# Performance work log

Hardware: AMD Instinct MI355X
Metric: run time of the kernel (lower is better)

Reference implementation:

```python
import jax, jax.numpy as jnp
import numpy as np
import math

HIDDEN = 2048
HEADS = 16
HEAD_DIM = HIDDEN // HEADS
SEQ = 2048
BATCH = 1
THRESH = 0.7


def setup_inputs() -> dict:
    key = jax.random.key(0)
    ks = jax.random.split(key, 9)
    init = lambda k, shape: (jax.random.normal(k, shape, dtype=jnp.float32) * 0.02)
    return {
        "hidden_states": jax.random.normal(ks[0], (BATCH, SEQ, HIDDEN), dtype=jnp.float32),
        "Wq": init(ks[1], (HIDDEN, HIDDEN)), "bq": jnp.zeros((HIDDEN,), jnp.float32),
        "Wk": init(ks[2], (HIDDEN, HIDDEN)), "bk": jnp.zeros((HIDDEN,), jnp.float32),
        "Wv": init(ks[3], (HIDDEN, HIDDEN)), "bv": jnp.zeros((HIDDEN,), jnp.float32),
        "Wo": init(ks[4], (HIDDEN, HIDDEN)), "bo": jnp.zeros((HIDDEN,), jnp.float32),
        "truth_gate": jnp.full((1,), THRESH, jnp.float32),
        "balance_gate": jnp.full((1,), THRESH, jnp.float32),
        "order_gate": jnp.full((1,), THRESH, jnp.float32),
        "justice_gate": jnp.full((1,), THRESH, jnp.float32),
        "harmony_gate": jnp.full((1,), THRESH, jnp.float32),
    }


def reference(hidden_states, Wq, bq, Wk, bk, Wv, bv, Wo, bo,
              truth_gate, balance_gate, order_gate, justice_gate, harmony_gate):
    B, S, D = hidden_states.shape
    H, hd = HEADS, HEAD_DIM
    # projections -> [B, H, S, hd]
    def proj(W, b):
        return (hidden_states @ W.T + b).reshape(B, S, H, hd).transpose(0, 2, 1, 3)
    q, k, v = proj(Wq, bq), proj(Wk, bk), proj(Wv, bv)

    scores = jnp.einsum('bhqd,bhkd->bhqk', q, k) / math.sqrt(hd)  # [B,H,S,S]

    # truth: penalize by key norm, broadcast over query axis? No -- k_norm is [B,H,S,1],
    # matching torch broadcasting: per-QUERY-row constant (k indexed like q rows).
    truth_penalty = jax.nn.sigmoid(truth_gate) * (jnp.linalg.norm(k, axis=-1, keepdims=True) * 0.01)

    # balance: row entropy of softmax(scores)
    logp = jax.nn.log_softmax(scores, axis=-1)
    entropy = -jnp.sum(jnp.exp(logp) * logp, axis=-1, keepdims=True)  # [B,H,S,1]
    balance_adjustment = jax.nn.sigmoid(balance_gate) * (entropy / math.log(S) * 0.1)

    # order: position bias over the LAST (key) axis, shape [1,1,S] in torch -> broadcasts on key dim
    position_bias = jnp.arange(S, dtype=jnp.float32) / S  # [S]
    order_bonus = jax.nn.sigmoid(order_gate) * (position_bias * 0.05)  # broadcasts over bhq,k

    # justice: pull scores toward their row mean
    mean_score = scores.mean(axis=-1, keepdims=True)
    justice_adjustment = jax.nn.sigmoid(justice_gate) * ((mean_score - scores) * 0.1)

    # harmony: negative mean abs diff along key axis, per row
    smoothness = -jnp.abs(scores[..., 1:] - scores[..., :-1]).mean(axis=-1, keepdims=True)
    harmony_smooth = jax.nn.sigmoid(harmony_gate) * (smoothness * 0.1)

    scores = scores - truth_penalty + balance_adjustment + order_bonus + justice_adjustment + harmony_smooth

    attn = jax.nn.softmax(scores, axis=-1)
    out = jnp.einsum('bhqk,bhkd->bhqd', attn, v)  # [B,H,S,hd]
    out = out.transpose(0, 2, 1, 3).reshape(B, S, D)
    return out @ Wo.T + bo
```

## Files before the change

### kernel.cpp

```cpp
#include <hip/hip_runtime.h>

typedef __bf16 bf16x8 __attribute__((ext_vector_type(8)));
typedef __bf16 bf16x4 __attribute__((ext_vector_type(4)));
typedef float f32x4 __attribute__((ext_vector_type(4)));

typedef const __attribute__((address_space(1))) void* gas_t;
typedef __attribute__((address_space(3))) void* las_t;

static constexpr int DIM = 2048;
static constexpr size_t MAT = (size_t)DIM * DIM;

__device__ __forceinline__ float sigmoidf_(float x) { return 1.f / (1.f + __expf(-x)); }

__global__ void cvt_kernel(const float* __restrict__ x, const float* __restrict__ wq,
                           const float* __restrict__ wk, const float* __restrict__ wv,
                           const float* __restrict__ wo, __bf16* __restrict__ dst) {
  const float* s;
  switch (blockIdx.y) {
    case 0: s = x; break;
    case 1: s = wq; break;
    case 2: s = wk; break;
    case 3: s = wv; break;
    default: s = wo; break;
  }
  __bf16* d = dst + (size_t)blockIdx.y * MAT;
  size_t i = ((size_t)blockIdx.x * 256 + threadIdx.x) * 4;
  float4 v = *(const float4*)(s + i);
  bf16x4 ov;
  ov[0] = (__bf16)v.x; ov[1] = (__bf16)v.y; ov[2] = (__bf16)v.z; ov[3] = (__bf16)v.w;
  *(bf16x4*)(d + i) = ov;
}

template <bool F32OUT>
__device__ __forceinline__ void gemm128(const __bf16* __restrict__ A, const __bf16* __restrict__ B,
                                        const float* __restrict__ bias, bool bias_row, float scale,
                                        void* __restrict__ Cout, int mtile, int ntile,
                                        __bf16* Asm, __bf16* Bsm) {
  const int t = threadIdx.x, lane = t & 63, w = t >> 6;
  const int wrow = (w >> 1) * 64, wcol = (w & 1) * 64;
  const int rbase = mtile * 128, cbase = ntile * 128;
  f32x4 acc[4][4] = {};

  for (int k0 = 0; k0 < DIM; k0 += 32) {
    __syncthreads();
#pragma unroll
    for (int i = 0; i < 2; ++i) {
      const int o = i * 4096 + w * 1024 + lane * 16;
      const int r = o >> 6;
      const int ke = (o & 63) >> 1;
      __builtin_amdgcn_global_load_lds((gas_t)(A + (size_t)(rbase + r) * DIM + k0 + ke),
                                       (las_t)(Asm + (o >> 1)), 16, 0, 0);
      __builtin_amdgcn_global_load_lds((gas_t)(B + (size_t)(cbase + r) * DIM + k0 + ke),
                                       (las_t)(Bsm + (o >> 1)), 16, 0, 0);
    }
    __syncthreads();

    bf16x8 af[4], bf[4];
#pragma unroll
    for (int i = 0; i < 4; ++i)
      af[i] = *(const bf16x8*)(Asm + (wrow + i * 16 + (lane & 15)) * 32 + (lane >> 4) * 8);
#pragma unroll
    for (int j = 0; j < 4; ++j)
      bf[j] = *(const bf16x8*)(Bsm + (wcol + j * 16 + (lane & 15)) * 32 + (lane >> 4) * 8);
#pragma unroll
    for (int i = 0; i < 4; ++i)
#pragma unroll
      for (int j = 0; j < 4; ++j)
        acc[i][j] = __builtin_amdgcn_mfma_f32_16x16x32_bf16(af[i], bf[j], acc[i][j], 0, 0, 0);
  }

#pragma unroll
  for (int i = 0; i < 4; ++i)
#pragma unroll
    for (int j = 0; j < 4; ++j)
#pragma unroll
      for (int r = 0; r < 4; ++r) {
        const int row = rbase + wrow + i * 16 + (lane >> 4) * 4 + r;
        const int col = cbase + wcol + j * 16 + (lane & 15);
        float v = acc[i][j][r] + (bias_row ? bias[row] : bias[col]);
        v *= scale;
        if (F32OUT)
          ((float*)Cout)[(size_t)row * DIM + col] = v;
        else
          ((__bf16*)Cout)[(size_t)row * DIM + col] = (__bf16)v;
      }
}

__global__ __launch_bounds__(256, 2) void qkv_kernel(
    const __bf16* __restrict__ Xb, const __bf16* __restrict__ Wqb, const __bf16* __restrict__ Wkb,
    const __bf16* __restrict__ Wvb, const float* __restrict__ bq, const float* __restrict__ bk,
    const float* __restrict__ bv, const float* __restrict__ jgate, __bf16* __restrict__ Qo,
    __bf16* __restrict__ Ko, __bf16* __restrict__ Vto) {
  __shared__ __bf16 Asm[128 * 32];
  __shared__ __bf16 Bsm[128 * 32];
  const int sel = blockIdx.x >> 4, nt = blockIdx.x & 15, mt = blockIdx.y;
  const __bf16 *A, *B;
  const float* bias;
  __bf16* C;
  bool brow = false;
  float sc = 1.f;
  if (sel == 0) {
    A = Xb; B = Wqb; bias = bq; C = Qo;
    sc = (1.f - 0.1f * sigmoidf_(jgate[0])) * 0.08838834764831843f;
  } else if (sel == 1) {
    A = Xb; B = Wkb; bias = bk; C = Ko;
  } else {
    A = Wvb; B = Xb; bias = bv; C = Vto; brow = true;
  }
  gemm128<false>(A, B, bias, brow, sc, C, mt, nt, Asm, Bsm);
}

__global__ __launch_bounds__(256, 2) void outproj_kernel(const __bf16* __restrict__ Ab,
                                                         const __bf16* __restrict__ Wob,
                                                         const float* __restrict__ bo,
                                                         float* __restrict__ Cout) {
  __shared__ __bf16 Asm[128 * 32];
  __shared__ __bf16 Bsm[128 * 32];
  gemm128<true>(Ab, Wob, bo, false, 1.f, Cout, blockIdx.y, blockIdx.x, Asm, Bsm);
}

__global__ __launch_bounds__(512) void attn_kernel(const __bf16* __restrict__ Q,
                                                   const __bf16* __restrict__ Kg,
                                                   const __bf16* __restrict__ VT,
                                                   const float* __restrict__ ogate,
                                                   __bf16* __restrict__ O) {
  __shared__ __bf16 Ks[2][4 * 64 * 32];
  __shared__ __bf16 Vs[2][2 * 128 * 32];
  __shared__ __bf16 Ps[8 * 16 * 72];
  const int t = threadIdx.x, lane = t & 63, w = t >> 6;
  const int h = blockIdx.y, qt = blockIdx.x;
  const float beta = sigmoidf_(ogate[0]) * 0.05f / 2048.0f;

  const int rs8 = (((lane >> 4) ^ ((lane >> 1) & 3)) & 3) * 8;

  const int qrow = qt * 128 + w * 16 + (lane & 15);
  bf16x8 qf[4];
#pragma unroll
  for (int c = 0; c < 4; ++c)
    qf[c] = *(const bf16x8*)(Q + (size_t)qrow * DIM + h * 128 + c * 32 + (lane >> 4) * 8);

  f32x4 oacc[8] = {};
  float m_r[4], l_r[4];
#pragma unroll
  for (int r = 0; r < 4; ++r) { m_r[r] = -1e30f; l_r[r] = 0.f; }

  auto stage = [&](int buf, int kt) {
#pragma unroll
    for (int i = 0; i < 2; ++i) {
      const int o = i * 8192 + w * 1024 + lane * 16;
      const int oz = o ^ (((o >> 7) & 3) << 4);
      const int ke = (oz & 63) >> 1;
      const int c = oz >> 12, key = (oz & 4095) >> 6;
      __builtin_amdgcn_global_load_lds(
          (gas_t)(Kg + (size_t)(kt + key) * DIM + h * 128 + c * 32 + ke),
          (las_t)(&Ks[buf][0] + (o >> 1)), 16, 0, 0);
      const int cc = oz >> 13, d = (oz & 8191) >> 6;
      __builtin_amdgcn_global_load_lds(
          (gas_t)(VT + (size_t)(h * 128 + d) * DIM + kt + cc * 32 + ke),
          (las_t)(&Vs[buf][0] + (o >> 1)), 16, 0, 0);
    }
  };

  stage(0, 0);
  int p = 0;
  for (int kt = 0; kt < 2048; kt += 64) {
    __syncthreads();
    if (kt + 64 < 2048) stage(p ^ 1, kt + 64);

    f32x4 s[4];
#pragma unroll
    for (int j = 0; j < 4; ++j) {
      f32x4 a = {};
#pragma unroll
      for (int c = 0; c < 4; ++c) {
        bf16x8 kf = *(const bf16x8*)(&Ks[p][0] + c * 2048 + (j * 16 + (lane & 15)) * 32 + rs8);
        a = __builtin_amdgcn_mfma_f32_16x16x32_bf16(qf[c], kf, a, 0, 0, 0);
      }
      s[j] = a;
    }
#pragma unroll
    for (int j = 0; j < 4; ++j) {
      const float pb = beta * (float)(kt + j * 16 + (lane & 15));
#pragma unroll
      for (int r = 0; r < 4; ++r) s[j][r] += pb;
    }
    float rmax[4];
#pragma unroll
    for (int r = 0; r < 4; ++r)
      rmax[r] = fmaxf(fmaxf(s[0][r], s[1][r]), fmaxf(s[2][r], s[3][r]));
#pragma unroll
    for (int msk = 1; msk < 16; msk <<= 1)
#pragma unroll
      for (int r = 0; r < 4; ++r) rmax[r] = fmaxf(rmax[r], __shfl_xor(rmax[r], msk, 64));

    float al[4];
#pragma unroll
    for (int r = 0; r < 4; ++r) {
      const float mn = fmaxf(m_r[r], rmax[r]);
      al[r] = __expf(m_r[r] - mn);
      m_r[r] = mn;
    }
#pragma unroll
    for (int j = 0; j < 4; ++j)
#pragma unroll
      for (int r = 0; r < 4; ++r) s[j][r] = __expf(s[j][r] - m_r[r]);

    float rs[4];
#pragma unroll
    for (int r = 0; r < 4; ++r) rs[r] = (s[0][r] + s[1][r]) + (s[2][r] + s[3][r]);
#pragma unroll
    for (int msk = 1; msk < 16; msk <<= 1)
#pragma unroll
      for (int r = 0; r < 4; ++r) rs[r] += __shfl_xor(rs[r], msk, 64);
#pragma unroll
    for (int r = 0; r < 4; ++r) l_r[r] = l_r[r] * al[r] + rs[r];
#pragma unroll
    for (int d = 0; d < 8; ++d)
#pragma unroll
      for (int r = 0; r < 4; ++r) oacc[d][r] *= al[r];

    {
      __bf16* pw = Ps + w * 1152;
#pragma unroll
      for (int j = 0; j < 4; ++j)
#pragma unroll
        for (int r = 0; r < 4; ++r)
          pw[((lane >> 4) * 4 + r) * 72 + j * 16 + (lane & 15)] = (__bf16)s[j][r];
    }

#pragma unroll
    for (int cc = 0; cc < 2; ++cc) {
      bf16x8 pa = *(const bf16x8*)(Ps + w * 1152 + (lane & 15) * 72 + cc * 32 + (lane >> 4) * 8);
#pragma unroll
      for (int d = 0; d < 8; ++d) {
        bf16x8 vf = *(const bf16x8*)(&Vs[p][0] + cc * 4096 + (d * 16 + (lane & 15)) * 32 + rs8);
        oacc[d] = __builtin_amdgcn_mfma_f32_16x16x32_bf16(pa, vf, oacc[d], 0, 0, 0);
      }
    }
    p ^= 1;
  }

#pragma unroll
  for (int d = 0; d < 8; ++d)
#pragma unroll
    for (int r = 0; r < 4; ++r) {
      const int row = qt * 128 + w * 16 + (lane >> 4) * 4 + r;
      const int col = h * 128 + d * 16 + (lane & 15);
      O[(size_t)row * DIM + col] = (__bf16)(oacc[d][r] / l_r[r]);
    }
}

extern "C" void kernel_launch(void* const* d_in, const int* in_sizes, int n_in,
                              void* d_out, int out_size, void* d_ws, size_t ws_size,
                              hipStream_t stream) {
  const float* X  = (const float*)d_in[0];
  const float* Wq = (const float*)d_in[1];
  const float* bq = (const float*)d_in[2];
  const float* Wk = (const float*)d_in[3];
  const float* bk = (const float*)d_in[4];
  const float* Wv = (const float*)d_in[5];
  const float* bv = (const float*)d_in[6];
  const float* Wo = (const float*)d_in[7];
  const float* bo = (const float*)d_in[8];
  const float* order_g   = (const float*)d_in[11];
  const float* justice_g = (const float*)d_in[12];

  __bf16* wsb = (__bf16*)d_ws;
  __bf16* Xb  = wsb + 0 * MAT;
  __bf16* Wqb = wsb + 1 * MAT;
  __bf16* Wkb = wsb + 2 * MAT;
  __bf16* Wvb = wsb + 3 * MAT;
  __bf16* Wob = wsb + 4 * MAT;
  __bf16* Qb  = wsb + 5 * MAT;
  __bf16* Kb  = wsb + 6 * MAT;
  __bf16* VTb = wsb + 7 * MAT;
  __bf16* Ab  = Xb;

  cvt_kernel<<<dim3(4096, 5), 256, 0, stream>>>(X, Wq, Wk, Wv, Wo, wsb);
  qkv_kernel<<<dim3(48, 16), 256, 0, stream>>>(Xb, Wqb, Wkb, Wvb, bq, bk, bv, justice_g,
                                               Qb, Kb, VTb);
  attn_kernel<<<dim3(16, 16), 512, 0, stream>>>(Qb, Kb, VTb, order_g, Ab);
  outproj_kernel<<<dim3(16, 16), 256, 0, stream>>>(Ab, Wob, bo, (float*)d_out);
}
```

Baseline: 315.5 us.

## Split attention over key halves with separate merge kernel

Splits the key sequence into two halves along a new grid dimension, doubling the attention grid from 256 to 512 blocks so the GPU's compute units are better occupied. Each half writes unnormalized fp32 partial outputs plus row max and sum, and a new merge kernel combines them into the bf16 attention output. It also swaps the padded P tile in shared memory for an XOR-swizzled layout. The cost is extra fp32 global traffic and an additional kernel launch. Partial buffers reuse the output buffer and workspace regions of weights that have already been consumed (Wq and Wv).

Result: no change. 318.1 us (+0.8%).

```diff
diff --git a/kernel.cpp b/kernel.cpp
--- a/kernel.cpp
+++ b/kernel.cpp
@@ -123,12 +123,15 @@
                                                    const __bf16* __restrict__ Kg,
                                                    const __bf16* __restrict__ VT,
                                                    const float* __restrict__ ogate,
-                                                   __bf16* __restrict__ O) {
+                                                   float* __restrict__ Od,
+                                                   float* __restrict__ Ow,
+                                                   float* __restrict__ ml) {
   __shared__ __bf16 Ks[2][4 * 64 * 32];
   __shared__ __bf16 Vs[2][2 * 128 * 32];
-  __shared__ __bf16 Ps[8 * 16 * 72];
+  __shared__ __bf16 Ps[8 * 16 * 64];
   const int t = threadIdx.x, lane = t & 63, w = t >> 6;
-  const int h = blockIdx.y, qt = blockIdx.x;
+  const int h = blockIdx.y, qt = blockIdx.x, s = blockIdx.z;
+  const int kt0 = s * 1024, kt1 = kt0 + 1024;
   const float beta = sigmoidf_(ogate[0]) * 0.05f / 2048.0f;
 
   const int rs8 = (((lane >> 4) ^ ((lane >> 1) & 3)) & 3) * 8;
@@ -154,20 +157,20 @@
       __builtin_amdgcn_global_load_lds(
           (gas_t)(Kg + (size_t)(kt + key) * DIM + h * 128 + c * 32 + ke),
           (las_t)(&Ks[buf][0] + (o >> 1)), 16, 0, 0);
-      const int cc = oz >> 13, d = (oz & 8191) >> 6;
+      const int d = (o & 8191) >> 6;
       __builtin_amdgcn_global_load_lds(
-          (gas_t)(VT + (size_t)(h * 128 + d) * DIM + kt + cc * 32 + ke),
+          (gas_t)(VT + (size_t)(h * 128 + d) * DIM + kt + i * 32 + ke),
           (las_t)(&Vs[buf][0] + (o >> 1)), 16, 0, 0);
     }
   };
 
-  stage(0, 0);
+  stage(0, kt0);
   int p = 0;
-  for (int kt = 0; kt < 2048; kt += 64) {
+  for (int kt = kt0; kt < kt1; kt += 64) {
     __syncthreads();
-    if (kt + 64 < 2048) stage(p ^ 1, kt + 64);
-
-    f32x4 s[4];
+    if (kt + 64 < kt1) stage(p ^ 1, kt + 64);
+
+    f32x4 sc[4];
 #pragma unroll
     for (int j = 0; j < 4; ++j) {
       f32x4 a = {};
@@ -176,18 +179,18 @@
         bf16x8 kf = *(const bf16x8*)(&Ks[p][0] + c * 2048 + (j * 16 + (lane & 15)) * 32 + rs8);
         a = __builtin_amdgcn_mfma_f32_16x16x32_bf16(qf[c], kf, a, 0, 0, 0);
       }
-      s[j] = a;
+      sc[j] = a;
     }
 #pragma unroll
     for (int j = 0; j < 4; ++j) {
       const float pb = beta * (float)(kt + j * 16 + (lane & 15));
 #pragma unroll
-      for (int r = 0; r < 4; ++r) s[j][r] += pb;
+      for (int r = 0; r < 4; ++r) sc[j][r] += pb;
     }
     float rmax[4];
 #pragma unroll
     for (int r = 0; r < 4; ++r)
-      rmax[r] = fmaxf(fmaxf(s[0][r], s[1][r]), fmaxf(s[2][r], s[3][r]));
+      rmax[r] = fmaxf(fmaxf(sc[0][r], sc[1][r]), fmaxf(sc[2][r], sc[3][r]));
 #pragma unroll
     for (int msk = 1; msk < 16; msk <<= 1)
 #pragma unroll
@@ -203,11 +206,11 @@
 #pragma unroll
     for (int j = 0; j < 4; ++j)
 #pragma unroll
-      for (int r = 0; r < 4; ++r) s[j][r] = __expf(s[j][r] - m_r[r]);
+      for (int r = 0; r < 4; ++r) sc[j][r] = __expf(sc[j][r] - m_r[r]);
 
     float rs[4];
 #pragma unroll
-    for (int r = 0; r < 4; ++r) rs[r] = (s[0][r] + s[1][r]) + (s[2][r] + s[3][r]);
+    for (int r = 0; r < 4; ++r) rs[r] = (sc[0][r] + sc[1][r]) + (sc[2][r] + sc[3][r]);
 #pragma unroll
     for (int msk = 1; msk < 16; msk <<= 1)
 #pragma unroll
@@ -220,17 +223,20 @@
       for (int r = 0; r < 4; ++r) oacc[d][r] *= al[r];
 
     {
-      __bf16* pw = Ps + w * 1152;
+      __bf16* pw = Ps + w * 1024;
 #pragma unroll
       for (int j = 0; j < 4; ++j)
 #pragma unroll
-        for (int r = 0; r < 4; ++r)
-          pw[((lane >> 4) * 4 + r) * 72 + j * 16 + (lane & 15)] = (__bf16)s[j][r];
+        for (int r = 0; r < 4; ++r) {
+          const int q = (lane >> 4) * 4 + r;
+          pw[(q * 64 + j * 16 + (lane & 15)) ^ ((q & 7) << 3)] = (__bf16)sc[j][r];
+        }
     }
 
 #pragma unroll
     for (int cc = 0; cc < 2; ++cc) {
-      bf16x8 pa = *(const bf16x8*)(Ps + w * 1152 + (lane & 15) * 72 + cc * 32 + (lane >> 4) * 8);
+      const int pe = (w * 1024 + (lane & 15) * 64 + cc * 32 + (lane >> 4) * 8) ^ ((lane & 7) << 3);
+      bf16x8 pa = *(const bf16x8*)(Ps + pe);
 #pragma unroll
       for (int d = 0; d < 8; ++d) {
         bf16x8 vf = *(const bf16x8*)(&Vs[p][0] + cc * 4096 + (d * 16 + (lane & 15)) * 32 + rs8);
@@ -240,14 +246,43 @@
     p ^= 1;
   }
 
+  float* Op = (s == 0) ? Od : Ow;
 #pragma unroll
   for (int d = 0; d < 8; ++d)
 #pragma unroll
     for (int r = 0; r < 4; ++r) {
       const int row = qt * 128 + w * 16 + (lane >> 4) * 4 + r;
       const int col = h * 128 + d * 16 + (lane & 15);
-      O[(size_t)row * DIM + col] = (__bf16)(oacc[d][r] / l_r[r]);
-    }
+      Op[(size_t)row * DIM + col] = oacc[d][r];
+    }
+  if ((lane & 15) == 0) {
+#pragma unroll
+    for (int r = 0; r < 4; ++r) {
+      const int row = qt * 128 + w * 16 + (lane >> 4) * 4 + r;
+      ml[s * 32768 + h * 2048 + row] = m_r[r];
+      ml[65536 + s * 32768 + h * 2048 + row] = l_r[r];
+    }
+  }
+}
+
+__global__ void merge_kernel(const float* __restrict__ O1, const float* __restrict__ O2,
+                             const float* __restrict__ ml, __bf16* __restrict__ Ab) {
+  const size_t i = ((size_t)blockIdx.x * 256 + threadIdx.x) * 4;
+  const int row = (int)(i >> 11), col = (int)(i & 2047), h = col >> 7;
+  const int mi = h * 2048 + row;
+  const float m1 = ml[mi], m2 = ml[32768 + mi];
+  const float l1 = ml[65536 + mi], l2 = ml[98304 + mi];
+  const float M = fmaxf(m1, m2);
+  const float a1 = __expf(m1 - M), a2 = __expf(m2 - M);
+  const float inv = 1.f / (a1 * l1 + a2 * l2);
+  const float4 o1 = *(const float4*)(O1 + i);
+  const float4 o2 = *(const float4*)(O2 + i);
+  bf16x4 ov;
+  ov[0] = (__bf16)((a1 * o1.x + a2 * o2.x) * inv);
+  ov[1] = (__bf16)((a1 * o1.y + a2 * o2.y) * inv);
+  ov[2] = (__bf16)((a1 * o1.z + a2 * o2.z) * inv);
+  ov[3] = (__bf16)((a1 * o1.w + a2 * o2.w) * inv);
+  *(bf16x4*)(Ab + i) = ov;
 }
 
 extern "C" void kernel_launch(void* const* d_in, const int* in_sizes, int n_in,
@@ -275,10 +310,14 @@
   __bf16* Kb  = wsb + 6 * MAT;
   __bf16* VTb = wsb + 7 * MAT;
   __bf16* Ab  = Xb;
+  float* Opart0 = (float*)d_out;
+  float* Opart1 = (float*)(wsb + 1 * MAT);
+  float* mlbuf  = (float*)(wsb + 3 * MAT);
 
   cvt_kernel<<<dim3(4096, 5), 256, 0, stream>>>(X, Wq, Wk, Wv, Wo, wsb);
   qkv_kernel<<<dim3(48, 16), 256, 0, stream>>>(Xb, Wqb, Wkb, Wvb, bq, bk, bv, justice_g,
                                                Qb, Kb, VTb);
-  attn_kernel<<<dim3(16, 16), 512, 0, stream>>>(Qb, Kb, VTb, order_g, Ab);
+  attn_kernel<<<dim3(16, 16, 2), 512, 0, stream>>>(Qb, Kb, VTb, order_g, Opart0, Opart1, mlbuf);
+  merge_kernel<<<dim3(4096), 256, 0, stream>>>(Opart0, Opart1, mlbuf, Ab);
   outproj_kernel<<<dim3(16, 16), 256, 0, stream>>>(Ab, Wob, bo, (float*)d_out);
 }
```

## Pipeline GEMM loads four-deep and streamline the attention softmax loop

Applied to the files above, without the earlier changes.

The shared 128x128 GEMM used by the QKV and output projections now keeps a four-buffer LDS ring. It issues async global-to-LDS loads three K-steps ahead and waits on explicit vmcnt counts with a single barrier per step, instead of load-then-sync every iteration. The attention kernel raises wave priority around its MFMA blocks and skips the running-max rescale when no row max increased. It also replaces the padded P scratch with an XOR-swizzled 64-wide layout to avoid LDS bank conflicts. The GEMM ring quadruples LDS per block, which may limit occupancy, and the hand-counted vmcnt waits depend on exactly four loads per stage.

New measurement: 360.9 us. +14.4%, slower.

```diff
diff --git a/kernel.cpp b/kernel.cpp
--- a/kernel.cpp
+++ b/kernel.cpp
@@ -41,32 +41,46 @@
   const int rbase = mtile * 128, cbase = ntile * 128;
   f32x4 acc[4][4] = {};
 
-  for (int k0 = 0; k0 < DIM; k0 += 32) {
-    __syncthreads();
+  auto stage = [&](int buf, int k0) {
 #pragma unroll
     for (int i = 0; i < 2; ++i) {
       const int o = i * 4096 + w * 1024 + lane * 16;
       const int r = o >> 6;
       const int ke = (o & 63) >> 1;
       __builtin_amdgcn_global_load_lds((gas_t)(A + (size_t)(rbase + r) * DIM + k0 + ke),
-                                       (las_t)(Asm + (o >> 1)), 16, 0, 0);
+                                       (las_t)(Asm + buf * 4096 + (o >> 1)), 16, 0, 0);
       __builtin_amdgcn_global_load_lds((gas_t)(B + (size_t)(cbase + r) * DIM + k0 + ke),
-                                       (las_t)(Bsm + (o >> 1)), 16, 0, 0);
-    }
-    __syncthreads();
+                                       (las_t)(Bsm + buf * 4096 + (o >> 1)), 16, 0, 0);
+    }
+  };
+
+  stage(0, 0);
+  stage(1, 32);
+  stage(2, 64);
+  int buf = 0;
+  for (int k0 = 0; k0 < DIM; k0 += 32) {
+    if (k0 + 64 < DIM)      asm volatile("s_waitcnt vmcnt(8)" ::: "memory");
+    else if (k0 + 32 < DIM) asm volatile("s_waitcnt vmcnt(4)" ::: "memory");
+    else                    asm volatile("s_waitcnt vmcnt(0)" ::: "memory");
+    __builtin_amdgcn_s_barrier();
+    if (k0 + 96 < DIM) {
+      int sb = buf + 3; if (sb >= 4) sb -= 4;
+      stage(sb, k0 + 96);
+    }
 
     bf16x8 af[4], bf[4];
 #pragma unroll
     for (int i = 0; i < 4; ++i)
-      af[i] = *(const bf16x8*)(Asm + (wrow + i * 16 + (lane & 15)) * 32 + (lane >> 4) * 8);
+      af[i] = *(const bf16x8*)(Asm + buf * 4096 + (wrow + i * 16 + (lane & 15)) * 32 + (lane >> 4) * 8);
 #pragma unroll
     for (int j = 0; j < 4; ++j)
-      bf[j] = *(const bf16x8*)(Bsm + (wcol + j * 16 + (lane & 15)) * 32 + (lane >> 4) * 8);
+      bf[j] = *(const bf16x8*)(Bsm + buf * 4096 + (wcol + j * 16 + (lane & 15)) * 32 + (lane >> 4) * 8);
 #pragma unroll
     for (int i = 0; i < 4; ++i)
 #pragma unroll
       for (int j = 0; j < 4; ++j)
         acc[i][j] = __builtin_amdgcn_mfma_f32_16x16x32_bf16(af[i], bf[j], acc[i][j], 0, 0, 0);
+    buf = (buf + 1) & 3;
   }
 
 #pragma unroll
@@ -91,8 +105,8 @@
     const __bf16* __restrict__ Wvb, const float* __restrict__ bq, const float* __restrict__ bk,
     const float* __restrict__ bv, const float* __restrict__ jgate, __bf16* __restrict__ Qo,
     __bf16* __restrict__ Ko, __bf16* __restrict__ Vto) {
-  __shared__ __bf16 Asm[128 * 32];
-  __shared__ __bf16 Bsm[128 * 32];
+  __shared__ __bf16 Asm[4 * 128 * 32];
+  __shared__ __bf16 Bsm[4 * 128 * 32];
   const int sel = blockIdx.x >> 4, nt = blockIdx.x & 15, mt = blockIdx.y;
   const __bf16 *A, *B;
   const float* bias;
@@ -114,8 +128,8 @@
                                                          const __bf16* __restrict__ Wob,
                                                          const float* __restrict__ bo,
                                                          float* __restrict__ Cout) {
-  __shared__ __bf16 Asm[128 * 32];
-  __shared__ __bf16 Bsm[128 * 32];
+  __shared__ __bf16 Asm[4 * 128 * 32];
+  __shared__ __bf16 Bsm[4 * 128 * 32];
   gemm128<true>(Ab, Wob, bo, false, 1.f, Cout, blockIdx.y, blockIdx.x, Asm, Bsm);
 }
 
@@ -126,7 +140,7 @@
                                                    __bf16* __restrict__ O) {
   __shared__ __bf16 Ks[2][4 * 64 * 32];
   __shared__ __bf16 Vs[2][2 * 128 * 32];
-  __shared__ __bf16 Ps[8 * 16 * 72];
+  __shared__ __bf16 Ps[8 * 16 * 64];
   const int t = threadIdx.x, lane = t & 63, w = t >> 6;
   const int h = blockIdx.y, qt = blockIdx.x;
   const float beta = sigmoidf_(ogate[0]) * 0.05f / 2048.0f;
@@ -154,9 +168,9 @@
       __builtin_amdgcn_global_load_lds(
           (gas_t)(Kg + (size_t)(kt + key) * DIM + h * 128 + c * 32 + ke),
           (las_t)(&Ks[buf][0] + (o >> 1)), 16, 0, 0);
-      const int cc = oz >> 13, d = (oz & 8191) >> 6;
+      const int d = (o & 8191) >> 6;
       __builtin_amdgcn_global_load_lds(
-          (gas_t)(VT + (size_t)(h * 128 + d) * DIM + kt + cc * 32 + ke),
+          (gas_t)(VT + (size_t)(h * 128 + d) * DIM + kt + i * 32 + ke),
           (las_t)(&Vs[buf][0] + (o >> 1)), 16, 0, 0);
     }
   };
@@ -167,7 +181,8 @@
     __syncthreads();
     if (kt + 64 < 2048) stage(p ^ 1, kt + 64);
 
-    f32x4 s[4];
+    __builtin_amdgcn_s_setprio(1);
+    f32x4 sc[4];
 #pragma unroll
     for (int j = 0; j < 4; ++j) {
       f32x4 a = {};
@@ -176,67 +191,75 @@
         bf16x8 kf = *(const bf16x8*)(&Ks[p][0] + c * 2048 + (j * 16 + (lane & 15)) * 32 + rs8);
         a = __builtin_amdgcn_mfma_f32_16x16x32_bf16(qf[c], kf, a, 0, 0, 0);
       }
-      s[j] = a;
-    }
+      sc[j] = a;
+    }
+    __builtin_amdgcn_s_setprio(0);
 #pragma unroll
     for (int j = 0; j < 4; ++j) {
       const float pb = beta * (float)(kt + j * 16 + (lane & 15));
 #pragma unroll
-      for (int r = 0; r < 4; ++r) s[j][r] += pb;
+      for (int r = 0; r < 4; ++r) sc[j][r] += pb;
     }
     float rmax[4];
 #pragma unroll
     for (int r = 0; r < 4; ++r)
-      rmax[r] = fmaxf(fmaxf(s[0][r], s[1][r]), fmaxf(s[2][r], s[3][r]));
+      rmax[r] = fmaxf(fmaxf(sc[0][r], sc[1][r]), fmaxf(sc[2][r], sc[3][r]));
 #pragma unroll
     for (int msk = 1; msk < 16; msk <<= 1)
 #pragma unroll
       for (int r = 0; r < 4; ++r) rmax[r] = fmaxf(rmax[r], __shfl_xor(rmax[r], msk, 64));
 
-    float al[4];
-#pragma unroll
-    for (int r = 0; r < 4; ++r) {
-      const float mn = fmaxf(m_r[r], rmax[r]);
-      al[r] = __expf(m_r[r] - mn);
-      m_r[r] = mn;
+    bool need = (rmax[0] > m_r[0]) | (rmax[1] > m_r[1]) |
+                (rmax[2] > m_r[2]) | (rmax[3] > m_r[3]);
+    if (__any(need)) {
+#pragma unroll
+      for (int r = 0; r < 4; ++r) {
+        const float mn = fmaxf(m_r[r], rmax[r]);
+        const float al = __expf(m_r[r] - mn);
+        m_r[r] = mn;
+        l_r[r] *= al;
+#pragma unroll
+        for (int d = 0; d < 8; ++d) oacc[d][r] *= al;
+      }
     }
 #pragma unroll
     for (int j = 0; j < 4; ++j)
 #pragma unroll
-      for (int r = 0; r < 4; ++r) s[j][r] = __expf(s[j][r] - m_r[r]);
+      for (int r = 0; r < 4; ++r) sc[j][r] = __expf(sc[j][r] - m_r[r]);
 
     float rs[4];
 #pragma unroll
-    for (int r = 0; r < 4; ++r) rs[r] = (s[0][r] + s[1][r]) + (s[2][r] + s[3][r]);
+    for (int r = 0; r < 4; ++r) rs[r] = (sc[0][r] + sc[1][r]) + (sc[2][r] + sc[3][r]);
 #pragma unroll
     for (int msk = 1; msk < 16; msk <<= 1)
 #pragma unroll
       for (int r = 0; r < 4; ++r) rs[r] += __shfl_xor(rs[r], msk, 64);
 #pragma unroll
-    for (int r = 0; r < 4; ++r) l_r[r] = l_r[r] * al[r] + rs[r];
-#pragma unroll
-    for (int d = 0; d < 8; ++d)
-#pragma unroll
-      for (int r = 0; r < 4; ++r) oacc[d][r] *= al[r];
+    for (int r = 0; r < 4; ++r) l_r[r] += rs[r];
 
     {
-      __bf16* pw = Ps + w * 1152;
+      __bf16* pw = Ps + w * 1024;
 #pragma unroll
       for (int j = 0; j < 4; ++j)
 #pragma unroll
-        for (int r = 0; r < 4; ++r)
-          pw[((lane >> 4) * 4 + r) * 72 + j * 16 + (lane & 15)] = (__bf16)s[j][r];
-    }
-
+        for (int r = 0; r < 4; ++r) {
+          const int q = (lane >> 4) * 4 + r;
+          pw[(q * 64 + j * 16 + (lane & 15)) ^ ((q & 7) << 3)] = (__bf16)sc[j][r];
+        }
+    }
+
+    __builtin_amdgcn_s_setprio(1);
 #pragma unroll
     for (int cc = 0; cc < 2; ++cc) {
-      bf16x8 pa = *(const bf16x8*)(Ps + w * 1152 + (lane & 15) * 72 + cc * 32 + (lane >> 4) * 8);
+      const int pe = (w * 1024 + (lane & 15) * 64 + cc * 32 + (lane >> 4) * 8) ^ ((lane & 7) << 3);
+      bf16x8 pa = *(const bf16x8*)(Ps + pe);
 #pragma unroll
       for (int d = 0; d < 8; ++d) {
         bf16x8 vf = *(const bf16x8*)(&Vs[p][0] + cc * 4096 + (d * 16 + (lane & 15)) * 32 + rs8);
         oacc[d] = __builtin_amdgcn_mfma_f32_16x16x32_bf16(pa, vf, oacc[d], 0, 0, 0);
       }
     }
+    __builtin_amdgcn_s_setprio(0);
     p ^= 1;
   }
 
```
